# Optimization experiments

Measured on AMD Instinct MI355X. Metric: run time of the kernel, lower is better.

Reference implementation:

```python
import jax, jax.numpy as jnp
import numpy as np

T = 5
V_TH = 0.5
GAMMA = 0.5
W_DECAY = 0.5
LOWER = 0.2 - 0.03
UPPER = 0.2 + 0.03
EMA_INIT = 0.17

@jax.custom_vjp
def sg_heaviside(x):
    return (x >= 0).astype(x.dtype)

def _sg_fwd(x):
    return sg_heaviside(x), x

def _sg_bwd(x, g):
    # grad_output * clamp(gamma - |x|, 0) / gamma^2  (triangular surrogate)
    return (g * jnp.clip(GAMMA - jnp.abs(x), 0.0) / (GAMMA * GAMMA),)

sg_heaviside.defvjp(_sg_fwd, _sg_bwd)


def setup_inputs() -> dict:
    key = jax.random.key(0)
    k1, k2 = jax.random.split(key)
    shape = (T, 32, 128, 32, 32)  # [T, B, C, H, W]
    x_exc = jax.random.uniform(k1, shape, dtype=jnp.float32)
    x_inh = jax.random.uniform(k2, shape, dtype=jnp.float32)
    alpha_raw = jnp.zeros((), dtype=jnp.float32)  # nn.Parameter alpha init 0.0
    beta_raw = jnp.zeros((), dtype=jnp.float32)   # nn.Parameter beta init 0.0
    return {"x_exc": x_exc, "x_inh": x_inh, "alpha_raw": alpha_raw, "beta_raw": beta_raw}


def reference(x_exc, x_inh, alpha_raw, beta_raw):
    beta = jax.nn.sigmoid(beta_raw)
    alpha = 4.0 * jax.nn.sigmoid(alpha_raw)
    B, C, H, W = x_exc.shape[1:]
    mem0 = jnp.zeros((B, C, H, W), x_exc.dtype)
    # ema starts constant 0.17 full-shape; after first mean it is [1,C,1,1].
    # Starting with [1,C,1,1] constant is mathematically identical.
    ema0 = jnp.full((1, C, 1, 1), EMA_INIT, x_exc.dtype)
    inhw0 = jnp.zeros((1, C, 1, 1), x_exc.dtype)

    def step(carry, xs):
        mem, ema, inhw = carry
        xe, xi = xs
        e_input = xe / (1.0 + alpha * xi)
        mem = W_DECAY * mem + e_input - beta * xi * (1.0 - inhw)
        spike = sg_heaviside(mem - V_TH)
        # ema update uses detached spikes; broadcasts [1,C,1,1]+[B,C,H,W] then means back
        ema = jnp.mean(0.9 * ema + 0.1 * jax.lax.stop_gradient(spike),
                       axis=(0, 2, 3), keepdims=True)
        # original only updates inh_weight for t < T-1, but the last update is
        # never read, so updating unconditionally is equivalent
        inhw = 4.0 * (jax.nn.sigmoid(LOWER - ema) - jax.nn.sigmoid(ema - UPPER))
        mem = mem - V_TH * spike
        return (mem, ema, inhw), spike

    _, spikes = jax.lax.scan(step, (mem0, ema0, inhw0), (x_exc, x_inh))
    return spikes  # [T, B, C, H, W]
```

## Files before the change

### kernel.cpp

```cpp
#include <hip/hip_runtime.h>

constexpr int T    = 5;
constexpr int Bn   = 32;
constexpr int C    = 128;
constexpr int HW   = 32 * 32;
constexpr int NPT4 = Bn * C * HW / 4;

constexpr int THREADS = 1024;
constexpr int WAVES   = THREADS / 64;
constexpr int BLOCKS  = 2 * C;
constexpr int K       = 8;

__global__ __launch_bounds__(THREADS)
void lif_kernel(const float* __restrict__ xe_g,
                const float* __restrict__ xi_g,
                const float* __restrict__ alpha_raw,
                const float* __restrict__ beta_raw,
                float* __restrict__ out) {
#pragma clang fp contract(off)
  const int blk  = blockIdx.x;
  const int c    = blk & (C - 1);
  const int half = blk >> 7;
  const int tid  = threadIdx.x;
  const int wave = tid >> 6;
  const int lane = tid & 63;

  __shared__ unsigned int wsum[T - 1][WAVES];

  const float alpha = 4.0f / (1.0f + expf(-alpha_raw[0]));
  const float beta  = 1.0f / (1.0f + expf(-beta_raw[0]));

  float mem[K][4];
#pragma unroll
  for (int k = 0; k < K; ++k)
#pragma unroll
    for (int j = 0; j < 4; ++j) mem[k][j] = 0.0f;

  float ema  = 0.17f;
  float inhw = 0.0f;

  const float4* xe4 = (const float4*)xe_g;
  const float4* xi4 = (const float4*)xi_g;
  float4*       o4  = (float4*)out;

  auto gidx = [&](int t, int k) -> size_t {
    const int b   = k * (THREADS / 256) + (tid >> 8);
    const int off = tid & 255;
    return (size_t)t * NPT4 + (size_t)(b * C + c) * 256 + off;
  };

  for (int t = 0; t < T; ++t) {
    float4 e4[K], i4[K];
#pragma unroll
    for (int k = 0; k < K; ++k) {
      const size_t idx = gidx(t, k);
      e4[k] = xe4[idx];
      i4[k] = xi4[idx];
    }

    unsigned int local = 0;
#pragma unroll
    for (int k = 0; k < K; ++k) {
      const float xe[4] = {e4[k].x, e4[k].y, e4[k].z, e4[k].w};
      const float xi[4] = {i4[k].x, i4[k].y, i4[k].z, i4[k].w};
      float sv[4];
#pragma unroll
      for (int j = 0; j < 4; ++j) {
        const float e_in = xe[j] / (1.0f + alpha * xi[j]);
        const float a  = 0.5f * mem[k][j];
        const float bb = a + e_in;
        const float d  = (beta * xi[j]) * (1.0f - inhw);
        const float m  = bb - d;
        const float x  = m - 0.5f;
        const float s  = (x >= 0.0f) ? 1.0f : 0.0f;
        local += (x >= 0.0f) ? 1u : 0u;
        mem[k][j] = m - 0.5f * s;
        sv[j] = s;
      }
      if ((k >> 2) == half) {
        float4 s4;
        s4.x = sv[0]; s4.y = sv[1]; s4.z = sv[2]; s4.w = sv[3];
        o4[gidx(t, k)] = s4;
      }
    }

    if (t == T - 1) break;

#pragma unroll
    for (int off = 32; off > 0; off >>= 1) local += __shfl_down(local, off);
    if (lane == 0) wsum[t][wave] = local;
    __syncthreads();
    unsigned int total = 0;
#pragma unroll
    for (int w = 0; w < WAVES; ++w) total += wsum[t][w];

    const float mean_spike = (float)total * (1.0f / 32768.0f);
    ema = 0.9f * ema + 0.1f * mean_spike;
    const float s_lo = 1.0f / (1.0f + expf(-(0.17f - ema)));
    const float s_hi = 1.0f / (1.0f + expf(-(ema - 0.23f)));
    inhw = 4.0f * (s_lo - s_hi);
  }
}

extern "C" void kernel_launch(void* const* d_in, const int* in_sizes, int n_in,
                              void* d_out, int out_size, void* d_ws, size_t ws_size,
                              hipStream_t stream) {
  const float* xe = (const float*)d_in[0];
  const float* xi = (const float*)d_in[1];
  const float* ar = (const float*)d_in[2];
  const float* br = (const float*)d_in[3];
  float* out = (float*)d_out;

  lif_kernel<<<dim3(BLOCKS), dim3(THREADS), 0, stream>>>(xe, xi, ar, br, out);
}
```

Baseline: 243.1 us.

## Split LIF scan into per-timestep launches with membrane state in workspace

Replaces the single fused kernel, which ran 256 blocks of 1024 threads with half of each block's work redundant, with five launches of 1024 blocks each, one per timestep. The membrane potential is carried between launches through a workspace buffer. Per-channel spike counts are written as partial sums that the next launch re-reduces to rebuild the EMA and inhibitory weight. The aim is to remove the redundant compute and raise occupancy, at the cost of extra membrane read/write traffic (about 64 MB per step) and launch boundaries. The old kernel is kept as a fallback when the workspace is too small.

```diff
diff --git a/kernel.cpp b/kernel.cpp
--- a/kernel.cpp
+++ b/kernel.cpp
@@ -1,99 +1,162 @@
 #include <hip/hip_runtime.h>
 
 constexpr int T    = 5;
-constexpr int Bn   = 32;
 constexpr int C    = 128;
-constexpr int HW   = 32 * 32;
-constexpr int NPT4 = Bn * C * HW / 4;
+constexpr int NPT4 = 32 * C * 1024 / 4;
 
-constexpr int THREADS = 1024;
-constexpr int WAVES   = THREADS / 64;
-constexpr int BLOCKS  = 2 * C;
-constexpr int K       = 8;
+constexpr int SBLOCKS  = 1024;
+constexpr int STHREADS = 256;
+constexpr int KT       = 4;
 
-__global__ __launch_bounds__(THREADS)
-void lif_kernel(const float* __restrict__ xe_g,
-                const float* __restrict__ xi_g,
-                const float* __restrict__ alpha_raw,
-                const float* __restrict__ beta_raw,
-                float* __restrict__ out) {
+constexpr size_t PART_BYTES = (size_t)T * SBLOCKS * sizeof(unsigned int);
+constexpr size_t WS_NEEDED  = PART_BYTES + (size_t)NPT4 * 16;
+
+__global__ __launch_bounds__(STHREADS)
+void lif_step(const float4* __restrict__ xe4,
+              const float4* __restrict__ xi4,
+              const float* __restrict__ alpha_raw,
+              const float* __restrict__ beta_raw,
+              float4* __restrict__ out4,
+              float4* __restrict__ memb,
+              unsigned int* __restrict__ partials,
+              int t) {
 #pragma clang fp contract(off)
-  const int blk  = blockIdx.x;
-  const int c    = blk & (C - 1);
-  const int half = blk >> 7;
-  const int tid  = threadIdx.x;
-  const int wave = tid >> 6;
-  const int lane = tid & 63;
+  const int blk = blockIdx.x;
+  const int tid = threadIdx.x;
+  const int c   = blk & (C - 1);
 
-  __shared__ unsigned int wsum[T - 1][WAVES];
-
+  __shared__ float s_inhw;
+  if (tid == 0) {
+    float inhw = 0.0f;
+    if (t > 0) {
+      float ema = 0.17f;
+      for (int s = 0; s < t; ++s) {
+        unsigned int tot = 0;
+#pragma unroll
+        for (int i = 0; i < 8; ++i) tot += partials[s * SBLOCKS + c + i * C];
+        const float mean = (float)tot * (1.0f / 32768.0f);
+        ema = 0.9f * ema + 0.1f * mean;
+      }
+      const float s_lo = 1.0f / (1.0f + expf(-(0.17f - ema)));
+      const float s_hi = 1.0f / (1.0f + expf(-(ema - 0.23f)));
+      inhw = 4.0f * (s_lo - s_hi);
+    }
+    s_inhw = inhw;
+  }
+  __syncthreads();
+  const float inhw  = s_inhw;
   const float alpha = 4.0f / (1.0f + expf(-alpha_raw[0]));
   const float beta  = 1.0f / (1.0f + expf(-beta_raw[0]));
 
-  float mem[K][4];
+  unsigned int local = 0;
+  const size_t tb = (size_t)t * NPT4;
 #pragma unroll
-  for (int k = 0; k < K; ++k)
+  for (int k = 0; k < KT; ++k) {
+    const size_t fi = (size_t)(k * SBLOCKS + blk) * 256 + tid;
+    const float4 e4 = xe4[tb + fi];
+    const float4 i4 = xi4[tb + fi];
+    float4 m4 = {0.0f, 0.0f, 0.0f, 0.0f};
+    if (t > 0) m4 = memb[fi];
+    const float xe[4] = {e4.x, e4.y, e4.z, e4.w};
+    const float xi[4] = {i4.x, i4.y, i4.z, i4.w};
+    float mv[4] = {m4.x, m4.y, m4.z, m4.w};
+    float sv[4];
+#pragma unroll
+    for (int j = 0; j < 4; ++j) {
+      const float e_in = xe[j] / (1.0f + alpha * xi[j]);
+      const float a  = 0.5f * mv[j];
+      const float bb = a + e_in;
+      const float d  = (beta * xi[j]) * (1.0f - inhw);
+      const float m  = bb - d;
+      const float x  = m - 0.5f;
+      const float s  = (x >= 0.0f) ? 1.0f : 0.0f;
+      local += (x >= 0.0f) ? 1u : 0u;
+      mv[j] = m - 0.5f * s;
+      sv[j] = s;
+    }
+    float4 s4; s4.x = sv[0]; s4.y = sv[1]; s4.z = sv[2]; s4.w = sv[3];
+    out4[tb + fi] = s4;
+    if (t < T - 1) {
+      float4 nm; nm.x = mv[0]; nm.y = mv[1]; nm.z = mv[2]; nm.w = mv[3];
+      memb[fi] = nm;
+    }
+  }
+
+  if (t < T - 1) {
+#pragma unroll
+    for (int off = 32; off > 0; off >>= 1) local += __shfl_down(local, off);
+    __shared__ unsigned int wsum[STHREADS / 64];
+    if ((tid & 63) == 0) wsum[tid >> 6] = local;
+    __syncthreads();
+    if (tid == 0)
+      partials[t * SBLOCKS + blk] = wsum[0] + wsum[1] + wsum[2] + wsum[3];
+  }
+}
+
+constexpr int FTHREADS = 1024;
+constexpr int FWAVES   = FTHREADS / 64;
+constexpr int FBLOCKS  = 2 * C;
+constexpr int FK       = 8;
+
+__global__ __launch_bounds__(FTHREADS)
+void lif_fallback(const float* __restrict__ xe_g, const float* __restrict__ xi_g,
+                  const float* __restrict__ alpha_raw,
+                  const float* __restrict__ beta_raw, float* __restrict__ out) {
+#pragma clang fp contract(off)
+  const int blk = blockIdx.x, c = blk & (C - 1), half = blk >> 7;
+  const int tid = threadIdx.x, wave = tid >> 6, lane = tid & 63;
+  __shared__ unsigned int wsum[T - 1][FWAVES];
+  const float alpha = 4.0f / (1.0f + expf(-alpha_raw[0]));
+  const float beta  = 1.0f / (1.0f + expf(-beta_raw[0]));
+  float mem[FK][4];
+#pragma unroll
+  for (int k = 0; k < FK; ++k)
 #pragma unroll
     for (int j = 0; j < 4; ++j) mem[k][j] = 0.0f;
-
-  float ema  = 0.17f;
-  float inhw = 0.0f;
-
+  float ema = 0.17f, inhw = 0.0f;
   const float4* xe4 = (const float4*)xe_g;
   const float4* xi4 = (const float4*)xi_g;
-  float4*       o4  = (float4*)out;
-
+  float4* o4 = (float4*)out;
   auto gidx = [&](int t, int k) -> size_t {
-    const int b   = k * (THREADS / 256) + (tid >> 8);
-    const int off = tid & 255;
-    return (size_t)t * NPT4 + (size_t)(b * C + c) * 256 + off;
+    const int b = k * (FTHREADS / 256) + (tid >> 8);
+    return (size_t)t * NPT4 + (size_t)(b * C + c) * 256 + (tid & 255);
   };
-
   for (int t = 0; t < T; ++t) {
-    float4 e4[K], i4[K];
+    float4 e4[FK], i4[FK];
 #pragma unroll
-    for (int k = 0; k < K; ++k) {
-      const size_t idx = gidx(t, k);
-      e4[k] = xe4[idx];
-      i4[k] = xi4[idx];
-    }
-
+    for (int k = 0; k < FK; ++k) { const size_t idx = gidx(t, k); e4[k] = xe4[idx]; i4[k] = xi4[idx]; }
     unsigned int local = 0;
 #pragma unroll
-    for (int k = 0; k < K; ++k) {
+    for (int k = 0; k < FK; ++k) {
       const float xe[4] = {e4[k].x, e4[k].y, e4[k].z, e4[k].w};
       const float xi[4] = {i4[k].x, i4[k].y, i4[k].z, i4[k].w};
       float sv[4];
 #pragma unroll
       for (int j = 0; j < 4; ++j) {
         const float e_in = xe[j] / (1.0f + alpha * xi[j]);
-        const float a  = 0.5f * mem[k][j];
+        const float a = 0.5f * mem[k][j];
         const float bb = a + e_in;
-        const float d  = (beta * xi[j]) * (1.0f - inhw);
-        const float m  = bb - d;
-        const float x  = m - 0.5f;
-        const float s  = (x >= 0.0f) ? 1.0f : 0.0f;
+        const float d = (beta * xi[j]) * (1.0f - inhw);
+        const float m = bb - d;
+        const float x = m - 0.5f;
+        const float s = (x >= 0.0f) ? 1.0f : 0.0f;
         local += (x >= 0.0f) ? 1u : 0u;
         mem[k][j] = m - 0.5f * s;
         sv[j] = s;
       }
       if ((k >> 2) == half) {
-        float4 s4;
-        s4.x = sv[0]; s4.y = sv[1]; s4.z = sv[2]; s4.w = sv[3];
+        float4 s4; s4.x = sv[0]; s4.y = sv[1]; s4.z = sv[2]; s4.w = sv[3];
         o4[gidx(t, k)] = s4;
       }
     }
-
     if (t == T - 1) break;
-
 #pragma unroll
     for (int off = 32; off > 0; off >>= 1) local += __shfl_down(local, off);
     if (lane == 0) wsum[t][wave] = local;
     __syncthreads();
     unsigned int total = 0;
 #pragma unroll
-    for (int w = 0; w < WAVES; ++w) total += wsum[t][w];
-
+    for (int w = 0; w < FWAVES; ++w) total += wsum[t][w];
     const float mean_spike = (float)total * (1.0f / 32768.0f);
     ema = 0.9f * ema + 0.1f * mean_spike;
     const float s_lo = 1.0f / (1.0f + expf(-(0.17f - ema)));
@@ -111,5 +174,16 @@
   const float* br = (const float*)d_in[3];
   float* out = (float*)d_out;
 
-  lif_kernel<<<dim3(BLOCKS), dim3(THREADS), 0, stream>>>(xe, xi, ar, br, out);
+  if (ws_size >= WS_NEEDED) {
+    unsigned int* partials = (unsigned int*)d_ws;
+    float4* memb = (float4*)((char*)d_ws + PART_BYTES);
+    const float4* xe4 = (const float4*)xe;
+    const float4* xi4 = (const float4*)xi;
+    float4* out4 = (float4*)out;
+    for (int t = 0; t < T; ++t)
+      lif_step<<<dim3(SBLOCKS), dim3(STHREADS), 0, stream>>>(
+          xe4, xi4, ar, br, out4, memb, partials, t);
+  } else {
+    lif_fallback<<<dim3(FBLOCKS), dim3(FTHREADS), 0, stream>>>(xe, xi, ar, br, out);
+  }
 }
```

Result: faster. 227.1 us (-6.6%).
